# Optimization experiments

Hardware: AMD Instinct MI355X
Metric: run time of the kernel (lower is better)

The kernel has to match this reference:

```python
import jax, jax.numpy as jnp
import numpy as np

B, T, V, H, E, F, NM = 128, 32, 10000, 512, 512, 2048, 512
D0 = E + NM + H   # 1536: layer-0 concat(x, h)
D1 = H + H        # 1024: layer-1 concat(h_prev_layer, h)


def setup_inputs() -> dict:
    key = jax.random.key(0)
    ks = jax.random.split(key, 10)
    cnn_features = jax.random.normal(ks[0], (B, F), jnp.float32)
    x_tokens = jax.random.randint(ks[1], (B, T), 0, V)
    current_hidden_state = jnp.zeros((2, B, 2 * H), jnp.float32)
    embedding = jax.random.normal(ks[2], (V, E), jnp.float32)
    W_in = jax.random.normal(ks[3], (F, NM), jnp.float32) / np.sqrt(F)
    b_in = jnp.zeros((NM,), jnp.float32)
    # 4 gates stacked (order: i, o, f, c) -- same math as 4 separate matmuls
    W0 = jax.random.normal(ks[4], (D0, 4 * H), jnp.float32) / np.sqrt(D0)
    b0 = jnp.full((4 * H,), 2.0, jnp.float32)
    W1 = jax.random.normal(ks[5], (D1, 4 * H), jnp.float32) / np.sqrt(D1)
    b1 = jnp.full((4 * H,), 2.0, jnp.float32)
    W_out = jax.random.normal(ks[6], (H, V), jnp.float32) / np.sqrt(H)
    b_out = jnp.zeros((V,), jnp.float32)
    return {"cnn_features": cnn_features, "x_tokens": x_tokens,
            "current_hidden_state": current_hidden_state, "embedding": embedding,
            "W_in": W_in, "b_in": b_in, "W0": W0, "b0": b0,
            "W1": W1, "b1": b1, "W_out": W_out, "b_out": b_out,
            "is_train": 1}


def _lstm_gates(z, c_prev):
    # gate order i, o, f, c matches the original cell's separate matmuls
    i_t, o_t, f_t, c_hat = jnp.split(z, 4, axis=1)
    i_t = jax.nn.sigmoid(i_t)
    o_t = jax.nn.sigmoid(o_t)
    f_t = jax.nn.sigmoid(f_t)
    c_hat = jnp.tanh(c_hat)
    c_t = f_t * c_prev + i_t * c_hat
    h_t = o_t * jnp.tanh(c_t)
    return h_t, c_t


def reference(cnn_features, x_tokens, current_hidden_state, embedding,
              W_in, b_in, W0, b0, W1, b1, W_out, b_out, is_train):
    # input_layer: Dropout (identity in eval) -> Linear -> LeakyReLU(0.01)
    proc = jax.nn.leaky_relu(cnn_features @ W_in + b_in, negative_slope=0.01)  # [B, NM]
    emb = embedding[x_tokens]  # [B, T, E] (teacher forcing: is_train=True)

    def step(hidden, emb_t):
        # layer 0: input = concat(token_emb, processed cnn features)
        x0 = jnp.concatenate([emb_t, proc], axis=1)          # [B, E+NM]
        h0, c0 = hidden[0, :, :H], hidden[0, :, H:]
        z0 = jnp.concatenate([x0, h0], axis=1) @ W0 + b0     # [B, 4H]
        h0n, c0n = _lstm_gates(z0, c0)
        # layer 1: input = h of layer 0 (already updated this timestep)
        h1, c1 = hidden[1, :, :H], hidden[1, :, H:]
        z1 = jnp.concatenate([h0n, h1], axis=1) @ W1 + b1    # [B, 4H]
        h1n, c1n = _lstm_gates(z1, c1)
        logits_t = h1n @ W_out + b_out                        # [B, V]
        new_hidden = jnp.stack([jnp.concatenate([h0n, c0n], axis=1),
                                jnp.concatenate([h1n, c1n], axis=1)], axis=0)
        return new_hidden, logits_t

    hidden, logits_seq = jax.lax.scan(step, current_hidden_state,
                                      jnp.moveaxis(emb, 1, 0))  # scan over T
    logits = jnp.moveaxis(logits_seq, 0, 1)  # [B, T, V]
    return logits, hidden
```

## Files before the change

kernel.cpp:

```cpp
#include <hip/hip_runtime.h>


typedef short s8v __attribute__((ext_vector_type(8)));
typedef float f4v __attribute__((ext_vector_type(4)));

#define OUT_H 40960000

__device__ __forceinline__ unsigned short f2bf(float f) {
  unsigned u = __float_as_uint(f);
  u += 0x7fffu + ((u >> 16) & 1u);
  return (unsigned short)(u >> 16);
}
__device__ __forceinline__ float sigm(float x) { return 1.0f / (1.0f + __expf(-x)); }
__device__ __forceinline__ float tanh_(float x) { return 1.0f - 2.0f / (1.0f + __expf(2.0f * x)); }

__device__ __forceinline__ void glds16(const unsigned short* g, unsigned short* l) {
  __builtin_amdgcn_global_load_lds((const __attribute__((address_space(1))) void*)g,
                                   (__attribute__((address_space(3))) void*)l, 16, 0, 0);
}

__global__ void k_transpose_cvt(const float* __restrict__ src, unsigned short* __restrict__ dst,
                                int R, int C) {
  __shared__ float tile[32][33];
  int c0 = blockIdx.x * 32, r0 = blockIdx.y * 32;
  int tx = threadIdx.x, ty = threadIdx.y;
#pragma unroll
  for (int i = 0; i < 4; i++) {
    int r = r0 + ty + i * 8, c = c0 + tx;
    if (r < R && c < C) tile[ty + i * 8][tx] = src[(size_t)r * C + c];
  }
  __syncthreads();
#pragma unroll
  for (int i = 0; i < 4; i++) {
    int c = c0 + ty + i * 8, r = r0 + tx;
    if (r < R && c < C) dst[(size_t)c * R + r] = f2bf(tile[tx][ty + i * 8]);
  }
}

__global__ void k_cvt_bf16(const float* __restrict__ in, unsigned short* __restrict__ out, int n4) {
  int i = blockIdx.x * 256 + threadIdx.x;
  if (i >= n4) return;
  float4 v = ((const float4*)in)[i];
  ushort4 p; p.x = f2bf(v.x); p.y = f2bf(v.y); p.z = f2bf(v.z); p.w = f2bf(v.w);
  ((ushort4*)out)[i] = p;
}

__global__ void k_gather_emb(const float* __restrict__ emb, const int* __restrict__ tok,
                             unsigned short* __restrict__ Xe) {
  int i = blockIdx.x * 256 + threadIdx.x;
  int r = i >> 7, k4 = (i & 127) * 4;
  int b = r & 127, t = r >> 7;
  int tk = tok[b * 32 + t];
  float4 v = *(const float4*)(emb + (size_t)tk * 512 + k4);
  ushort4 p; p.x = f2bf(v.x); p.y = f2bf(v.y); p.z = f2bf(v.z); p.w = f2bf(v.w);
  ((ushort4*)Xe)[i] = p;
}

__global__ void k_init2(const float* __restrict__ chs,
                        unsigned short* __restrict__ h0b1, unsigned short* __restrict__ h1b1,
                        int* __restrict__ bar) {
  int i = blockIdx.x * 256 + threadIdx.x;
  int b = i >> 9, j = i & 511;
  h0b1[i] = f2bf(chs[b * 1024 + j]);
  h1b1[i] = f2bf(chs[131072 + b * 1024 + j]);
  if (i < 4096) bar[i] = 0;
}

template <int MODE>
__global__ __launch_bounds__(256, 2)
void k_gemm(const unsigned short* __restrict__ A, const unsigned short* __restrict__ Bt,
            const float* __restrict__ bias, const float* __restrict__ add128,
            float* __restrict__ outF, unsigned short* __restrict__ outB,
            int M, int N, int K) {
  __shared__ unsigned short As[4096];
  __shared__ unsigned short Bs[4096];
  int tid = threadIdx.x;
  int wave = tid >> 6, lane = tid & 63;
  int lr = lane & 15, lq = lane >> 4;
  int wm = (wave >> 1) * 64, wn = (wave & 1) * 64;
  int m0 = blockIdx.y * 128, n0 = blockIdx.x * 128;

  f4v acc[4][4];
  f4v zero = {0.0f, 0.0f, 0.0f, 0.0f};
#pragma unroll
  for (int i = 0; i < 4; i++)
#pragma unroll
    for (int j = 0; j < 4; j++) acc[i][j] = zero;

  int srow = tid >> 2, sofs = (tid & 3) * 8;
  int ar0 = m0 + srow, ar1 = ar0 + 64;
  int br0 = n0 + srow, br1 = br0 + 64;
  if (br0 >= N) br0 = N - 1;
  if (br1 >= N) br1 = N - 1;
  const unsigned short* Ag0 = A + (size_t)ar0 * K + sofs;
  const unsigned short* Ag1 = A + (size_t)ar1 * K + sofs;
  const unsigned short* Bg0 = Bt + (size_t)br0 * K + sofs;
  const unsigned short* Bg1 = Bt + (size_t)br1 * K + sofs;
  unsigned short* lA0 = &As[tid * 8];
  unsigned short* lA1 = &As[2048 + tid * 8];
  unsigned short* lB0 = &Bs[tid * 8];
  unsigned short* lB1 = &Bs[2048 + tid * 8];

  for (int k0 = 0; k0 < K; k0 += 32) {
    glds16(Ag0 + k0, lA0);
    glds16(Ag1 + k0, lA1);
    glds16(Bg0 + k0, lB0);
    glds16(Bg1 + k0, lB1);
    __syncthreads();
    s8v af[4], bfr[4];
#pragma unroll
    for (int i = 0; i < 4; i++) af[i] = *(const s8v*)&As[(wm + i * 16 + lr) * 32 + lq * 8];
#pragma unroll
    for (int i = 0; i < 4; i++) bfr[i] = *(const s8v*)&Bs[(wn + i * 16 + lr) * 32 + lq * 8];
#pragma unroll
    for (int i = 0; i < 4; i++)
#pragma unroll
      for (int j = 0; j < 4; j++)
        acc[i][j] = __builtin_amdgcn_mfma_f32_16x16x32_bf16(af[i], bfr[j], acc[i][j], 0, 0, 0);
    __syncthreads();
  }

#pragma unroll
  for (int i = 0; i < 4; i++) {
#pragma unroll
    for (int j = 0; j < 4; j++) {
      int nn = n0 + wn + j * 16 + lr;
      if (nn >= N) continue;
#pragma unroll
      for (int r = 0; r < 4; r++) {
        int mm = m0 + wm + i * 16 + lq * 4 + r;
        float v = acc[i][j][r];
        if (MODE == 0) {
          v += bias[nn];
          v = v > 0.0f ? v : 0.01f * v;
          outB[(size_t)mm * N + nn] = f2bf(v);
        } else if (MODE == 1) {
          v += bias[nn];
          outF[(size_t)mm * N + nn] = v;
        } else if (MODE == 2) {
          v += add128[(size_t)(mm & 127) * N + nn];
          outF[(size_t)mm * N + nn] = v;
        } else {
          v += bias[nn];
          int b = mm & 127, t = mm >> 7;
          outF[(size_t)(b * 32 + t) * N + nn] = v;
        }
      }
    }
  }
}

template <int NKC>
__device__ __forceinline__ void pmm(const unsigned short* __restrict__ hA,
                                    const unsigned short* __restrict__ w0,
                                    const unsigned short* __restrict__ w1,
                                    const unsigned short* __restrict__ w2,
                                    const unsigned short* __restrict__ w3,
                                    int am0, int am1, int ko, f4v acc[2][4]) {
#pragma unroll
  for (int kc = 0; kc < NKC; kc++) {
    int kk = kc * 32 + ko;
    s8v a0 = *(const s8v*)(hA + am0 * 512 + kk);
    s8v a1 = *(const s8v*)(hA + am1 * 512 + kk);
    s8v b0 = *(const s8v*)(w0 + kk);
    s8v b1 = *(const s8v*)(w1 + kk);
    s8v b2 = *(const s8v*)(w2 + kk);
    s8v b3 = *(const s8v*)(w3 + kk);
    acc[0][0] = __builtin_amdgcn_mfma_f32_16x16x32_bf16(a0, b0, acc[0][0], 0, 0, 0);
    acc[1][0] = __builtin_amdgcn_mfma_f32_16x16x32_bf16(a1, b0, acc[1][0], 0, 0, 0);
    acc[0][1] = __builtin_amdgcn_mfma_f32_16x16x32_bf16(a0, b1, acc[0][1], 0, 0, 0);
    acc[1][1] = __builtin_amdgcn_mfma_f32_16x16x32_bf16(a1, b1, acc[1][1], 0, 0, 0);
    acc[0][2] = __builtin_amdgcn_mfma_f32_16x16x32_bf16(a0, b2, acc[0][2], 0, 0, 0);
    acc[1][2] = __builtin_amdgcn_mfma_f32_16x16x32_bf16(a1, b2, acc[1][2], 0, 0, 0);
    acc[0][3] = __builtin_amdgcn_mfma_f32_16x16x32_bf16(a0, b3, acc[0][3], 0, 0, 0);
    acc[1][3] = __builtin_amdgcn_mfma_f32_16x16x32_bf16(a1, b3, acc[1][3], 0, 0, 0);
  }
}

__device__ __forceinline__ void gridbar(int* bar, int gen) {
  __syncthreads();
  if (threadIdx.x == 0) {
    __threadfence();
    __hip_atomic_store(&bar[blockIdx.x * 16], gen, __ATOMIC_RELAXED, __HIP_MEMORY_SCOPE_AGENT);
  }
  while (__hip_atomic_load(&bar[threadIdx.x * 16], __ATOMIC_RELAXED, __HIP_MEMORY_SCOPE_AGENT) < gen) {}
  __syncthreads();
  if (threadIdx.x == 0) __threadfence();
  __syncthreads();
}

__global__ __launch_bounds__(256, 2)
void k_lstm(const unsigned short* __restrict__ W0h_t, const unsigned short* __restrict__ W1_t,
            const float* __restrict__ Zx, const float* __restrict__ b1,
            const float* __restrict__ chs,
            unsigned short* __restrict__ h0b0, unsigned short* __restrict__ h0b1,
            unsigned short* __restrict__ h1b0, unsigned short* __restrict__ h1b1,
            unsigned short* __restrict__ H1all, float* __restrict__ outHid,
            int* __restrict__ bar) {
  __shared__ f4v part[8][4][64];
  int tid = threadIdx.x;
  int wave = tid >> 6, lane = tid & 63;
  int lr = lane & 15, lq = lane >> 4;
  int bb = blockIdx.x;
  bool isB = bb < 128;
  int gb = isB ? bb : bb - 128;
  int jt = gb >> 2, mh = gb & 3;
  int kq = wave;
  int j = jt * 16 + lr;
  int Kfull = isB ? 1024 : 512;
  int kbase = kq * (Kfull >> 2);
  int am0 = (mh * 2) * 16 + lr;
  int am1 = (mh * 2 + 1) * 16 + lr;
  int me_base = (mh * 2 + wave) * 16 + lq * 4;

  const unsigned short* Wt = isB ? W1_t : W0h_t;
  const unsigned short* wg0 = Wt + (size_t)(0 * 512 + jt * 16 + lr) * Kfull + kbase;
  const unsigned short* wg1 = Wt + (size_t)(1 * 512 + jt * 16 + lr) * Kfull + kbase;
  const unsigned short* wg2 = Wt + (size_t)(2 * 512 + jt * 16 + lr) * Kfull + kbase;
  const unsigned short* wg3 = Wt + (size_t)(3 * 512 + jt * 16 + lr) * Kfull + kbase;

  float cs[4] = {0, 0, 0, 0};
  float bi = 0, bo = 0, bf_ = 0, bc = 0;
  if (wave < 2) {
    int coff = isB ? 131072 : 0;
#pragma unroll
    for (int r = 0; r < 4; r++) cs[r] = chs[coff + (size_t)(me_base + r) * 1024 + 512 + j];
    if (isB) { bi = b1[j]; bo = b1[512 + j]; bf_ = b1[1024 + j]; bc = b1[1536 + j]; }
  }

  for (int p = 0; p <= 32; p++) {
    int t = isB ? (p - 1) : p;
    bool active = isB ? (p >= 1) : (p <= 31);
    f4v acc[2][4];
    if (active) {
      const unsigned short* hA;
      if (isB) {
        const unsigned short* h0r = (t & 1) ? h0b1 : h0b0;
        const unsigned short* h1r = (t & 1) ? h1b0 : h1b1;
        hA = (kbase < 512) ? (h0r + kbase) : (h1r + kbase - 512);
      } else {
        hA = ((t & 1) ? h0b0 : h0b1) + kbase;
      }
      f4v zero = {0.0f, 0.0f, 0.0f, 0.0f};
#pragma unroll
      for (int i = 0; i < 2; i++)
#pragma unroll
        for (int g = 0; g < 4; g++) acc[i][g] = zero;
      if (isB) pmm<8>(hA, wg0, wg1, wg2, wg3, am0, am1, lq * 8, acc);
      else     pmm<4>(hA, wg0, wg1, wg2, wg3, am0, am1, lq * 8, acc);
#pragma unroll
      for (int i = 0; i < 2; i++)
#pragma unroll
        for (int g = 0; g < 4; g++) part[kq * 2 + i][g][lane] = acc[i][g];
    }
    __syncthreads();
    if (active && wave < 2) {
      f4v z[4];
#pragma unroll
      for (int g = 0; g < 4; g++) {
        f4v s = part[wave][g][lane];
        s += part[2 + wave][g][lane];
        s += part[4 + wave][g][lane];
        s += part[6 + wave][g][lane];
        z[g] = s;
      }
      unsigned short* hw;
      if (isB) hw = (t & 1) ? h1b1 : h1b0;
      else     hw = (t & 1) ? h0b1 : h0b0;
#pragma unroll
      for (int r = 0; r < 4; r++) {
        int m = me_base + r;
        float zi, zo, zf, zc;
        if (isB) {
          zi = z[0][r] + bi; zo = z[1][r] + bo; zf = z[2][r] + bf_; zc = z[3][r] + bc;
        } else {
          const float* zrow = Zx + (size_t)t * 262144 + (size_t)m * 2048;
          zi = z[0][r] + zrow[j];        zo = z[1][r] + zrow[512 + j];
          zf = z[2][r] + zrow[1024 + j]; zc = z[3][r] + zrow[1536 + j];
        }
        float iv = sigm(zi), ov = sigm(zo), fv = sigm(zf), cv = tanh_(zc);
        float cn = fv * cs[r] + iv * cv;
        float hn = ov * tanh_(cn);
        cs[r] = cn;
        unsigned short hb = f2bf(hn);
        hw[m * 512 + j] = hb;
        if (isB) H1all[((size_t)t * 128 + m) * 512 + j] = hb;
        if (t == 31) {
          size_t o = OUT_H + (isB ? 131072 : 0) + (size_t)m * 1024;
          outHid[o + j] = hn;
          outHid[o + 512 + j] = cn;
        }
      }
    }
    if (p < 32) gridbar(bar, p + 1);
  }
}

extern "C" void kernel_launch(void* const* d_in, const int* in_sizes, int n_in,
                              void* d_out, int out_size, void* d_ws, size_t ws_size,
                              hipStream_t stream) {
  const float* cnn  = (const float*)d_in[0];
  const int*   tok  = (const int*)d_in[1];
  const float* chs  = (const float*)d_in[2];
  const float* emb  = (const float*)d_in[3];
  const float* W_in = (const float*)d_in[4];
  const float* b_in = (const float*)d_in[5];
  const float* W0   = (const float*)d_in[6];
  const float* b0   = (const float*)d_in[7];
  const float* W1   = (const float*)d_in[8];
  const float* b1   = (const float*)d_in[9];
  const float* W_out= (const float*)d_in[10];
  const float* b_out= (const float*)d_in[11];
  float* out = (float*)d_out;

  char* p = (char*)d_ws;
  auto alloc = [&](size_t bytes) { char* q = p; p += (bytes + 255) & ~(size_t)255; return q; };
  unsigned short* Win_t  = (unsigned short*)alloc((size_t)512 * 2048 * 2);
  unsigned short* W0e_t  = (unsigned short*)alloc((size_t)2048 * 512 * 2);
  unsigned short* W0m_t  = (unsigned short*)alloc((size_t)2048 * 512 * 2);
  unsigned short* W0h_t  = (unsigned short*)alloc((size_t)2048 * 512 * 2);
  unsigned short* W1_t   = (unsigned short*)alloc((size_t)2048 * 1024 * 2);
  unsigned short* Wout_t = (unsigned short*)alloc((size_t)10000 * 512 * 2);
  unsigned short* cnn_b  = (unsigned short*)alloc((size_t)128 * 2048 * 2);
  unsigned short* proc_b = (unsigned short*)alloc((size_t)128 * 512 * 2);
  float*          Cf     = (float*)alloc((size_t)128 * 2048 * 4);
  unsigned short* Xe     = (unsigned short*)alloc((size_t)4096 * 512 * 2);
  float*          Zx     = (float*)alloc((size_t)4096 * 2048 * 4);
  unsigned short* h0b0   = (unsigned short*)alloc(65536 * 2);
  unsigned short* h0b1   = (unsigned short*)alloc(65536 * 2);
  unsigned short* h1b0   = (unsigned short*)alloc(65536 * 2);
  unsigned short* h1b1   = (unsigned short*)alloc(65536 * 2);
  unsigned short* H1all  = (unsigned short*)alloc((size_t)4096 * 512 * 2);
  int*            bar    = (int*)alloc(4096 * 4);

  dim3 tb(32, 8);
  k_transpose_cvt<<<dim3(16, 64),  tb, 0, stream>>>(W_in, Win_t, 2048, 512);
  k_transpose_cvt<<<dim3(64, 16),  tb, 0, stream>>>(W0,               W0e_t, 512, 2048);
  k_transpose_cvt<<<dim3(64, 16),  tb, 0, stream>>>(W0 + 512 * 2048,  W0m_t, 512, 2048);
  k_transpose_cvt<<<dim3(64, 16),  tb, 0, stream>>>(W0 + 1024 * 2048, W0h_t, 512, 2048);
  k_transpose_cvt<<<dim3(64, 32),  tb, 0, stream>>>(W1, W1_t, 1024, 2048);
  k_transpose_cvt<<<dim3(313, 16), tb, 0, stream>>>(W_out, Wout_t, 512, 10000);
  k_cvt_bf16<<<256, 256, 0, stream>>>(cnn, cnn_b, 65536);

  k_gemm<0><<<dim3(4, 1), 256, 0, stream>>>(cnn_b, Win_t, b_in, nullptr, nullptr, proc_b,
                                            128, 512, 2048);
  k_gemm<1><<<dim3(16, 1), 256, 0, stream>>>(proc_b, W0m_t, b0, nullptr, Cf, nullptr,
                                             128, 2048, 512);
  k_gather_emb<<<2048, 256, 0, stream>>>(emb, tok, Xe);
  k_gemm<2><<<dim3(16, 32), 256, 0, stream>>>(Xe, W0e_t, nullptr, Cf, Zx, nullptr,
                                              4096, 2048, 512);
  k_init2<<<256, 256, 0, stream>>>(chs, h0b1, h1b1, bar);

  k_lstm<<<256, 256, 0, stream>>>(W0h_t, W1_t, Zx, b1, chs,
                                  h0b0, h0b1, h1b0, h1b1, H1all, out, bar);

  k_gemm<3><<<dim3(79, 32), 256, 0, stream>>>(H1all, Wout_t, b_out, nullptr, out, nullptr,
                                              4096, 10000, 512);
}
```

Baseline: 992.6 us.

## Replace grid-barrier fences with atomic fp32 hidden-state exchange

The persistent LSTM kernel's grid barrier drops its __threadfence calls and adds s_sleep in the spin loop. To keep the hidden state visible across blocks without fences, the ping-pong h buffers become fp32 and are written and read with relaxed agent-scope atomics, with bf16 conversion done on load. This removes fence cost at each of the 32 step barriers, but doubles h-buffer traffic, adds conversion work to the inner matmul loads, and relies on relaxed atomics alone for ordering, which may be weaker than the fences it replaces.

```diff
diff --git a/kernel.cpp b/kernel.cpp
--- a/kernel.cpp
+++ b/kernel.cpp
@@ -17,6 +17,21 @@
 __device__ __forceinline__ void glds16(const unsigned short* g, unsigned short* l) {
   __builtin_amdgcn_global_load_lds((const __attribute__((address_space(1))) void*)g,
                                    (__attribute__((address_space(3))) void*)l, 16, 0, 0);
+}
+
+__device__ __forceinline__ s8v load_h8(const float* p) {
+  unsigned long long q[4];
+#pragma unroll
+  for (int i = 0; i < 4; i++)
+    q[i] = __hip_atomic_load((const unsigned long long*)p + i,
+                             __ATOMIC_RELAXED, __HIP_MEMORY_SCOPE_AGENT);
+  s8v r;
+#pragma unroll
+  for (int i = 0; i < 4; i++) {
+    r[2 * i]     = (short)f2bf(__uint_as_float((unsigned)(q[i] & 0xffffffffull)));
+    r[2 * i + 1] = (short)f2bf(__uint_as_float((unsigned)(q[i] >> 32)));
+  }
+  return r;
 }
 
 __global__ void k_transpose_cvt(const float* __restrict__ src, unsigned short* __restrict__ dst,
@@ -57,12 +72,12 @@
 }
 
 __global__ void k_init2(const float* __restrict__ chs,
-                        unsigned short* __restrict__ h0b1, unsigned short* __restrict__ h1b1,
+                        float* __restrict__ h0b1, float* __restrict__ h1b1,
                         int* __restrict__ bar) {
   int i = blockIdx.x * 256 + threadIdx.x;
   int b = i >> 9, j = i & 511;
-  h0b1[i] = f2bf(chs[b * 1024 + j]);
-  h1b1[i] = f2bf(chs[131072 + b * 1024 + j]);
+  h0b1[i] = chs[b * 1024 + j];
+  h1b1[i] = chs[131072 + b * 1024 + j];
   if (i < 4096) bar[i] = 0;
 }
 
@@ -151,7 +166,7 @@
 }
 
 template <int NKC>
-__device__ __forceinline__ void pmm(const unsigned short* __restrict__ hA,
+__device__ __forceinline__ void pmm(const float* __restrict__ hA,
                                     const unsigned short* __restrict__ w0,
                                     const unsigned short* __restrict__ w1,
                                     const unsigned short* __restrict__ w2,
@@ -160,8 +175,8 @@
 #pragma unroll
   for (int kc = 0; kc < NKC; kc++) {
     int kk = kc * 32 + ko;
-    s8v a0 = *(const s8v*)(hA + am0 * 512 + kk);
-    s8v a1 = *(const s8v*)(hA + am1 * 512 + kk);
+    s8v a0 = load_h8(hA + am0 * 512 + kk);
+    s8v a1 = load_h8(hA + am1 * 512 + kk);
     s8v b0 = *(const s8v*)(w0 + kk);
     s8v b1 = *(const s8v*)(w1 + kk);
     s8v b2 = *(const s8v*)(w2 + kk);
@@ -179,13 +194,11 @@
 
 __device__ __forceinline__ void gridbar(int* bar, int gen) {
   __syncthreads();
-  if (threadIdx.x == 0) {
-    __threadfence();
+  if (threadIdx.x == 0)
     __hip_atomic_store(&bar[blockIdx.x * 16], gen, __ATOMIC_RELAXED, __HIP_MEMORY_SCOPE_AGENT);
-  }
-  while (__hip_atomic_load(&bar[threadIdx.x * 16], __ATOMIC_RELAXED, __HIP_MEMORY_SCOPE_AGENT) < gen) {}
-  __syncthreads();
-  if (threadIdx.x == 0) __threadfence();
+  while (__hip_atomic_load(&bar[threadIdx.x * 16], __ATOMIC_RELAXED,
+                           __HIP_MEMORY_SCOPE_AGENT) < gen)
+    __builtin_amdgcn_s_sleep(1);
   __syncthreads();
 }
 
@@ -193,8 +206,8 @@
 void k_lstm(const unsigned short* __restrict__ W0h_t, const unsigned short* __restrict__ W1_t,
             const float* __restrict__ Zx, const float* __restrict__ b1,
             const float* __restrict__ chs,
-            unsigned short* __restrict__ h0b0, unsigned short* __restrict__ h0b1,
-            unsigned short* __restrict__ h1b0, unsigned short* __restrict__ h1b1,
+            float* __restrict__ h0b0, float* __restrict__ h0b1,
+            float* __restrict__ h1b0, float* __restrict__ h1b1,
             unsigned short* __restrict__ H1all, float* __restrict__ outHid,
             int* __restrict__ bar) {
   __shared__ f4v part[8][4][64];
@@ -233,10 +246,10 @@
     bool active = isB ? (p >= 1) : (p <= 31);
     f4v acc[2][4];
     if (active) {
-      const unsigned short* hA;
+      const float* hA;
       if (isB) {
-        const unsigned short* h0r = (t & 1) ? h0b1 : h0b0;
-        const unsigned short* h1r = (t & 1) ? h1b0 : h1b1;
+        const float* h0r = (t & 1) ? h0b1 : h0b0;
+        const float* h1r = (t & 1) ? h1b0 : h1b1;
         hA = (kbase < 512) ? (h0r + kbase) : (h1r + kbase - 512);
       } else {
         hA = ((t & 1) ? h0b0 : h0b1) + kbase;
@@ -264,7 +277,7 @@
         s += part[6 + wave][g][lane];
         z[g] = s;
       }
-      unsigned short* hw;
+      float* hw;
       if (isB) hw = (t & 1) ? h1b1 : h1b0;
       else     hw = (t & 1) ? h0b1 : h0b0;
 #pragma unroll
@@ -282,9 +295,8 @@
         float cn = fv * cs[r] + iv * cv;
         float hn = ov * tanh_(cn);
         cs[r] = cn;
-        unsigned short hb = f2bf(hn);
-        hw[m * 512 + j] = hb;
-        if (isB) H1all[((size_t)t * 128 + m) * 512 + j] = hb;
+        __hip_atomic_store(&hw[m * 512 + j], hn, __ATOMIC_RELAXED, __HIP_MEMORY_SCOPE_AGENT);
+        if (isB) H1all[((size_t)t * 128 + m) * 512 + j] = f2bf(hn);
         if (t == 31) {
           size_t o = OUT_H + (isB ? 131072 : 0) + (size_t)m * 1024;
           outHid[o + j] = hn;
@@ -326,10 +338,10 @@
   float*          Cf     = (float*)alloc((size_t)128 * 2048 * 4);
   unsigned short* Xe     = (unsigned short*)alloc((size_t)4096 * 512 * 2);
   float*          Zx     = (float*)alloc((size_t)4096 * 2048 * 4);
-  unsigned short* h0b0   = (unsigned short*)alloc(65536 * 2);
-  unsigned short* h0b1   = (unsigned short*)alloc(65536 * 2);
-  unsigned short* h1b0   = (unsigned short*)alloc(65536 * 2);
-  unsigned short* h1b1   = (unsigned short*)alloc(65536 * 2);
+  float*          h0b0   = (float*)alloc(65536 * 4);
+  float*          h0b1   = (float*)alloc(65536 * 4);
+  float*          h1b0   = (float*)alloc(65536 * 4);
+  float*          h1b1   = (float*)alloc(65536 * 4);
   unsigned short* H1all  = (unsigned short*)alloc((size_t)4096 * 512 * 2);
   int*            bar    = (int*)alloc(4096 * 4);
 
```

Result: faster. 873.1 us (-12.0%).
